# Performance work log

Measured on AMD Instinct MI355X. Metric: run time of the kernel, lower is better.

Reference implementation:

```python
import jax, jax.numpy as jnp
import numpy as np

NUM_GRAPHS = 1024


def setup_inputs() -> dict:
    key = jax.random.key(0)
    k1, k2, k3, k4 = jax.random.split(key, 4)
    N, D, H = 500000, 256, 128
    x = jax.random.normal(k1, (N, D), dtype=jnp.float32)
    # attention MLP params (Linear(D,H) -> ReLU -> Linear(H,1))
    W1 = jax.random.normal(k2, (D, H), dtype=jnp.float32) * (1.0 / np.sqrt(D))
    b1 = jnp.zeros((H,), dtype=jnp.float32)
    W2 = jax.random.normal(k3, (H, 1), dtype=jnp.float32) * (1.0 / np.sqrt(H))
    b2 = jnp.zeros((1,), dtype=jnp.float32)
    batch = jnp.sort(jax.random.randint(k4, (N,), 0, NUM_GRAPHS)).astype(jnp.int64)
    return {"x": x, "W1": W1, "b1": b1, "W2": W2, "b2": b2, "batch": batch}


def reference(x, W1, b1, W2, b2, batch):
    # attention MLP -> scalar score per node, softmax over ALL nodes (global, as in source)
    h = jax.nn.relu(x @ W1 + b1)            # [N, H]
    scores = h @ W2 + b2                    # [N, 1]
    attn = jax.nn.softmax(scores.ravel())[:, None]  # [N, 1], global softmax

    # attention-weighted sum per graph
    attn_pooled = jax.ops.segment_sum(x * attn, batch, num_segments=NUM_GRAPHS,
                                      indices_are_sorted=True)  # [G, D]
    # max pool per graph (all segments occupied given N >> G)
    max_pooled = jax.ops.segment_max(x, batch, num_segments=NUM_GRAPHS,
                                     indices_are_sorted=True)   # [G, D]
    # mean pool per graph: scatter-add + clamped counts
    sum_pooled = jax.ops.segment_sum(x, batch, num_segments=NUM_GRAPHS,
                                     indices_are_sorted=True)   # [G, D]
    counts = jnp.bincount(batch, length=NUM_GRAPHS).astype(x.dtype)
    counts = jnp.clip(counts, 1.0, None)[:, None]                # [G, 1]
    mean_pooled = sum_pooled / counts

    return jnp.concatenate([attn_pooled, max_pooled, mean_pooled], axis=-1)  # [G, 3D]
```

## Files before the change

### kernel.cpp

```cpp
#include <hip/hip_runtime.h>
#include <cmath>

#define D_IN 256
#define H_DIM 128
#define NUM_GRAPHS 1024
#define CHUNK 64
#define MAXSEG 4
#define REC_F 768

typedef __attribute__((ext_vector_type(8))) __bf16 bf16x8;
typedef __attribute__((ext_vector_type(4))) float f32x4;
typedef __attribute__((ext_vector_type(4))) unsigned short ushort4v;

__device__ inline float b2f(unsigned short u) {
    unsigned int v = ((unsigned int)u) << 16;
    return __builtin_bit_cast(float, v);
}

__global__ void pack_w1(const float* __restrict__ W1, ushort* __restrict__ packed) {
    int tid = blockIdx.x * 256 + threadIdx.x;
    if (tid >= 8 * 8 * 64) return;
    int nt = tid >> 9;
    int ks = (tid >> 6) & 7;
    int l = tid & 63;
    int col = nt * 16 + (l & 15);
    int kbase = ks * 32 + ((l >> 4) & 3) * 8;
#pragma unroll
    for (int i = 0; i < 8; ++i) {
        float v = W1[(size_t)(kbase + i) * H_DIM + col];
        __bf16 b = (__bf16)v;
        packed[(size_t)tid * 8 + i] = __builtin_bit_cast(unsigned short, b);
    }
}

__global__ __launch_bounds__(256) void fused_kernel(
    const float* __restrict__ x, const ushort* __restrict__ w1p,
    const float* __restrict__ b1, const float* __restrict__ W2,
    const float* __restrict__ b2, const int* __restrict__ batch,
    float* __restrict__ recs, int2* __restrict__ hdr,
    float* __restrict__ zpart, int N) {
    int tid = threadIdx.x;
    int l = tid & 63;
    int w = tid >> 6;
    int r16 = l & 15;
    int kg = l >> 4;
    int blk = blockIdx.x;
    long long base = (long long)blk * CHUNK;
    int chunkN = (int)min((long long)CHUNK, (long long)N - base);

    __shared__ ushort sx[CHUNK * D_IN];
    __shared__ float pscore[CHUNK][4];
    __shared__ float red[4][3][256];
    __shared__ int sbatch[CHUNK];
    __shared__ int seglist[MAXSEG + 1];
    __shared__ int seggid[MAXSEG];
    __shared__ int snseg;

    int bval = 0;
    if (w == 0) {
        long long bi = base + l;
        bval = (bi < N) ? batch[bi] : -1;
        sbatch[l] = bval;
    }

    bf16x8 breg0[8], breg1[8];
#pragma unroll
    for (int ks = 0; ks < 8; ++ks) {
        breg0[ks] = *(const bf16x8*)(w1p + ((size_t)((w * 2) * 8 + ks) * 64 + l) * 8);
        breg1[ks] = *(const bf16x8*)(w1p + ((size_t)((w * 2 + 1) * 8 + ks) * 64 + l) * 8);
    }

    {
        int row = tid >> 2;
        long long grow = base + row;
        if (grow >= N) grow = N - 1;
        const float* xr = x + grow * D_IN;
        int gb = tid & 3;
        f32x4 xv[16];
#pragma unroll
        for (int j = 0; j < 8; ++j) {
            int g = gb + 4 * j;
            xv[2 * j] = *(const f32x4*)(xr + g * 8);
            xv[2 * j + 1] = *(const f32x4*)(xr + g * 8 + 4);
        }
        unsigned rowswz = (unsigned)(row & 7) << 4;
#pragma unroll
        for (int j = 0; j < 8; ++j) {
            int g = gb + 4 * j;
            bf16x8 pk;
#pragma unroll
            for (int i = 0; i < 4; ++i) {
                pk[i] = (__bf16)xv[2 * j][i];
                pk[i + 4] = (__bf16)xv[2 * j + 1][i];
            }
            unsigned addr = ((unsigned)(row * 512 + g * 16)) ^ rowswz;
            *(bf16x8*)((char*)sx + addr) = pk;
        }
    }

    float w2v[2], b1v[2];
#pragma unroll
    for (int q = 0; q < 2; ++q) {
        int c = (w * 2 + q) * 16 + r16;
        w2v[q] = W2[c];
        b1v[q] = b1[c];
    }
    float bb = b2[0];

    if (w == 0) {
        int prev = __shfl_up(bval, 1, 64);
        bool flag = (l < chunkN) && (l == 0 || bval != prev);
        unsigned long long m = __ballot(flag);
        if (l == 0) {
            int ns = 0;
            while (m && ns < MAXSEG) {
                int b = __ffsll(m) - 1;
                seglist[ns] = b;
                seggid[ns] = sbatch[b];
                ns++;
                m &= m - 1;
            }
            snseg = ns;
            seglist[ns] = chunkN;
        }
    }
    __syncthreads();

    f32x4 acc[4][2] = {};
#pragma unroll
    for (int ks = 0; ks < 8; ++ks) {
#pragma unroll
        for (int mt = 0; mt < 4; ++mt) {
            int row = mt * 16 + r16;
            unsigned addr = ((unsigned)(row * 512 + ks * 64 + kg * 16)) ^
                            ((unsigned)(row & 7) << 4);
            bf16x8 af = *(const bf16x8*)((const char*)sx + addr);
            acc[mt][0] = __builtin_amdgcn_mfma_f32_16x16x32_bf16(af, breg0[ks], acc[mt][0], 0, 0, 0);
            acc[mt][1] = __builtin_amdgcn_mfma_f32_16x16x32_bf16(af, breg1[ks], acc[mt][1], 0, 0, 0);
        }
    }
#pragma unroll
    for (int mt = 0; mt < 4; ++mt) {
#pragma unroll
        for (int reg = 0; reg < 4; ++reg) {
            float p = fmaxf(acc[mt][0][reg] + b1v[0], 0.f) * w2v[0] +
                      fmaxf(acc[mt][1][reg] + b1v[1], 0.f) * w2v[1];
            p += __shfl_xor(p, 1, 64);
            p += __shfl_xor(p, 2, 64);
            p += __shfl_xor(p, 4, 64);
            p += __shfl_xor(p, 8, 64);
            if (r16 == 0) pscore[mt * 16 + kg * 4 + reg][w] = p;
        }
    }
    __syncthreads();

    f32x4 ps = *(const f32x4*)&pscore[l][0];
    float e_l = (l < chunkN) ? __expf(ps[0] + ps[1] + ps[2] + ps[3] + bb) : 0.f;

    if (w == 0) {
        float z = e_l;
        z += __shfl_xor(z, 1, 64);
        z += __shfl_xor(z, 2, 64);
        z += __shfl_xor(z, 4, 64);
        z += __shfl_xor(z, 8, 64);
        z += __shfl_xor(z, 16, 64);
        z += __shfl_xor(z, 32, 64);
        if (l == 0) zpart[blk] = z;
    }

    int nseg = snseg;

    f32x4 asum = {0.f, 0.f, 0.f, 0.f};
    f32x4 ssum = {0.f, 0.f, 0.f, 0.f};
    f32x4 mx = {-INFINITY, -INFINITY, -INFINITY, -INFINITY};

    for (int sg = 0; sg < nseg; ++sg) {
        int sStart = seglist[sg];
        int sEnd = seglist[sg + 1];
#pragma unroll
        for (int j = 0; j < 16; ++j) {
            int row = w * 16 + j;
            float wj = __shfl(e_l, row, 64);
            bool in = (row >= sStart) && (row < sEnd);
            unsigned addr = ((unsigned)(row * 512 + l * 8)) ^
                            ((unsigned)(row & 7) << 4);
            ushort4v hv = *(const ushort4v*)((const char*)sx + addr);
            float wje = in ? wj : 0.f;
#pragma unroll
            for (int c = 0; c < 4; ++c) {
                float v = b2f(hv[c]);
                asum[c] += v * wje;
                ssum[c] += in ? v : 0.f;
                mx[c] = fmaxf(mx[c], in ? v : -INFINITY);
            }
        }
        *(f32x4*)&red[w][0][l * 4] = asum;
        *(f32x4*)&red[w][1][l * 4] = ssum;
        *(f32x4*)&red[w][2][l * 4] = mx;
        __syncthreads();
        {
            float aa = red[0][0][tid] + red[1][0][tid] +
                       red[2][0][tid] + red[3][0][tid];
            float s2 = red[0][1][tid] + red[1][1][tid] +
                       red[2][1][tid] + red[3][1][tid];
            float m2 = fmaxf(fmaxf(red[0][2][tid], red[1][2][tid]),
                             fmaxf(red[2][2][tid], red[3][2][tid]));
            float* rb = recs + (size_t)(blk * MAXSEG + sg) * REC_F;
            rb[tid] = aa;
            rb[256 + tid] = s2;
            rb[512 + tid] = m2;
        }
        if (tid == 0)
            hdr[blk * MAXSEG + sg] = make_int2(seggid[sg], sEnd - sStart);
        __syncthreads();
#pragma unroll
        for (int c = 0; c < 4; ++c) {
            asum[c] = 0.f;
            ssum[c] = 0.f;
            mx[c] = -INFINITY;
        }
    }
    if (tid == 0) {
        for (int sg = nseg; sg < MAXSEG; ++sg)
            hdr[blk * MAXSEG + sg] = make_int2(-1, 0);
    }
}

__global__ __launch_bounds__(256) void zreduce_kernel(
    const float* __restrict__ zpart, int n, float* __restrict__ MZ) {
    int tid = threadIdx.x;
    float z = 0.f;
    for (int i = tid; i < n; i += 256) z += zpart[i];
    __shared__ float sz[256];
    sz[tid] = z;
    __syncthreads();
    for (int off = 128; off > 0; off >>= 1) {
        if (tid < off) sz[tid] += sz[tid + off];
        __syncthreads();
    }
    if (tid == 0) MZ[0] = 1.f / sz[0];
}

__device__ inline int lower_bound_i(const int* __restrict__ arr, int n, int val) {
    int lo = 0, hi = n;
    while (lo < hi) {
        int mid = (lo + hi) >> 1;
        if (arr[mid] < val) lo = mid + 1; else hi = mid;
    }
    return lo;
}

__global__ __launch_bounds__(256) void combine_kernel(
    const float* __restrict__ recs, const int2* __restrict__ hdr,
    const float* __restrict__ MZ,
    const int* __restrict__ batch, int N, float* __restrict__ out) {
    int g = blockIdx.x;
    int tid = threadIdx.x;
    float invZ = MZ[0];

    __shared__ int sb[2];
    if (tid < 2) sb[tid] = lower_bound_i(batch, N, g + tid);
    __syncthreads();
    int start = sb[0], end = sb[1];

    float ew = 0.f, ss = 0.f, mxv = -INFINITY;
    int cnt = 0;
    if (end > start) {
        int b0 = start >> 6, b1 = (end - 1) >> 6;
        for (int b = b0; b <= b1; ++b) {
#pragma unroll
            for (int sg = 0; sg < MAXSEG; ++sg) {
                int2 h = hdr[b * MAXSEG + sg];
                if (h.x == g) {
                    const float* rb = recs + (size_t)(b * MAXSEG + sg) * REC_F;
                    ew += rb[tid];
                    ss += rb[256 + tid];
                    mxv = fmaxf(mxv, rb[512 + tid]);
                    cnt += h.y;
                }
            }
        }
    }
    size_t ob = (size_t)g * (3 * D_IN);
    out[ob + tid] = ew * invZ;
    out[ob + D_IN + tid] = (end > start) ? mxv : 0.f;
    out[ob + 2 * D_IN + tid] = ss / (float)max(cnt, 1);
}

extern "C" void kernel_launch(void* const* d_in, const int* in_sizes, int n_in,
                              void* d_out, int out_size, void* d_ws, size_t ws_size,
                              hipStream_t stream) {
    const float* x = (const float*)d_in[0];
    const float* W1 = (const float*)d_in[1];
    const float* b1 = (const float*)d_in[2];
    const float* W2 = (const float*)d_in[3];
    const float* b2 = (const float*)d_in[4];
    const int* batch = (const int*)d_in[5];
    int N = in_sizes[0] / D_IN;
    float* out = (float*)d_out;
    int NB = (N + CHUNK - 1) / CHUNK;

    char* ws = (char*)d_ws;
    size_t off = 0;
    ushort* w1p = (ushort*)(ws + off);
    off += 8 * 8 * 64 * 8 * sizeof(ushort);
    off = (off + 255) & ~(size_t)255;
    float* recs = (float*)(ws + off);
    off += (size_t)NB * MAXSEG * REC_F * sizeof(float);
    off = (off + 255) & ~(size_t)255;
    int2* hdr = (int2*)(ws + off);
    off += (size_t)NB * MAXSEG * sizeof(int2);
    off = (off + 255) & ~(size_t)255;
    float* zpart = (float*)(ws + off);
    off += (size_t)NB * sizeof(float);
    off = (off + 255) & ~(size_t)255;
    float* MZ = (float*)(ws + off);
    off += 256;

    pack_w1<<<16, 256, 0, stream>>>(W1, w1p);
    fused_kernel<<<NB, 256, 0, stream>>>(x, w1p, b1, W2, b2, batch,
                                         recs, hdr, zpart, N);
    zreduce_kernel<<<1, 256, 0, stream>>>(zpart, NB, MZ);
    combine_kernel<<<NUM_GRAPHS, 256, 0, stream>>>(recs, hdr, MZ, batch, N, out);
}
```

Before: 181.3 us.

## Reduce segment pooling within each wave via shuffles and precompute graph bounds

The per-segment pooling loop now assigns each wave a 64-column slice, with the four 16-lane row groups reduced through cross-lane shuffles. This replaces the shared-memory red buffer and the two block barriers per segment. The per-block segment header array is dropped. A fused prep kernel precomputes the graph boundaries and each chunk's first graph id, so combine indexes records directly instead of doing a binary search and a header scan. This removes LDS traffic, barriers and redundant searches, but it relies on chunk segment ids being contiguous starting from cfirst.

```diff
diff --git a/kernel.cpp b/kernel.cpp
--- a/kernel.cpp
+++ b/kernel.cpp
@@ -17,19 +17,39 @@
     return __builtin_bit_cast(float, v);
 }
 
-__global__ void pack_w1(const float* __restrict__ W1, ushort* __restrict__ packed) {
-    int tid = blockIdx.x * 256 + threadIdx.x;
-    if (tid >= 8 * 8 * 64) return;
-    int nt = tid >> 9;
-    int ks = (tid >> 6) & 7;
-    int l = tid & 63;
-    int col = nt * 16 + (l & 15);
-    int kbase = ks * 32 + ((l >> 4) & 3) * 8;
-#pragma unroll
-    for (int i = 0; i < 8; ++i) {
-        float v = W1[(size_t)(kbase + i) * H_DIM + col];
-        __bf16 b = (__bf16)v;
-        packed[(size_t)tid * 8 + i] = __builtin_bit_cast(unsigned short, b);
+__device__ inline int lower_bound_i(const int* __restrict__ arr, int n, int val) {
+    int lo = 0, hi = n;
+    while (lo < hi) {
+        int mid = (lo + hi) >> 1;
+        if (arr[mid] < val) lo = mid + 1; else hi = mid;
+    }
+    return lo;
+}
+
+__global__ __launch_bounds__(256) void prep_kernel(
+    const float* __restrict__ W1, const int* __restrict__ batch, int N, int NB,
+    ushort* __restrict__ packed, int* __restrict__ bounds,
+    int* __restrict__ cfirst) {
+    int b = blockIdx.x;
+    if (b < 16) {
+        int tid = b * 256 + threadIdx.x;
+        int nt = tid >> 9;
+        int ks = (tid >> 6) & 7;
+        int l = tid & 63;
+        int col = nt * 16 + (l & 15);
+        int kbase = ks * 32 + ((l >> 4) & 3) * 8;
+#pragma unroll
+        for (int i = 0; i < 8; ++i) {
+            float v = W1[(size_t)(kbase + i) * H_DIM + col];
+            __bf16 h = (__bf16)v;
+            packed[(size_t)tid * 8 + i] = __builtin_bit_cast(unsigned short, h);
+        }
+    } else if (b < 21) {
+        int i = (b - 16) * 256 + threadIdx.x;
+        if (i <= NUM_GRAPHS) bounds[i] = lower_bound_i(batch, N, i);
+    } else {
+        int i = (b - 21) * 256 + threadIdx.x;
+        if (i < NB) cfirst[i] = batch[(long long)i * CHUNK];
     }
 }
 
@@ -37,8 +57,7 @@
     const float* __restrict__ x, const ushort* __restrict__ w1p,
     const float* __restrict__ b1, const float* __restrict__ W2,
     const float* __restrict__ b2, const int* __restrict__ batch,
-    float* __restrict__ recs, int2* __restrict__ hdr,
-    float* __restrict__ zpart, int N) {
+    float* __restrict__ recs, float* __restrict__ zpart, int N) {
     int tid = threadIdx.x;
     int l = tid & 63;
     int w = tid >> 6;
@@ -49,18 +68,14 @@
     int chunkN = (int)min((long long)CHUNK, (long long)N - base);
 
     __shared__ ushort sx[CHUNK * D_IN];
-    __shared__ float pscore[CHUNK][4];
-    __shared__ float red[4][3][256];
-    __shared__ int sbatch[CHUNK];
+    __shared__ float pscore[4][CHUNK];
     __shared__ int seglist[MAXSEG + 1];
-    __shared__ int seggid[MAXSEG];
     __shared__ int snseg;
 
-    int bval = 0;
+    int bval = -1;
     if (w == 0) {
         long long bi = base + l;
         bval = (bi < N) ? batch[bi] : -1;
-        sbatch[l] = bval;
     }
 
     bf16x8 breg0[8], breg1[8];
@@ -116,7 +131,6 @@
             while (m && ns < MAXSEG) {
                 int b = __ffsll(m) - 1;
                 seglist[ns] = b;
-                seggid[ns] = sbatch[b];
                 ns++;
                 m &= m - 1;
             }
@@ -149,13 +163,13 @@
             p += __shfl_xor(p, 2, 64);
             p += __shfl_xor(p, 4, 64);
             p += __shfl_xor(p, 8, 64);
-            if (r16 == 0) pscore[mt * 16 + kg * 4 + reg][w] = p;
+            if (r16 == 0) pscore[w][mt * 16 + kg * 4 + reg] = p;
         }
     }
     __syncthreads();
 
-    f32x4 ps = *(const f32x4*)&pscore[l][0];
-    float e_l = (l < chunkN) ? __expf(ps[0] + ps[1] + ps[2] + ps[3] + bb) : 0.f;
+    float s = pscore[0][l] + pscore[1][l] + pscore[2][l] + pscore[3][l] + bb;
+    float e_l = (l < chunkN) ? __expf(s) : 0.f;
 
     if (w == 0) {
         float z = e_l;
@@ -170,19 +184,22 @@
 
     int nseg = snseg;
 
-    f32x4 asum = {0.f, 0.f, 0.f, 0.f};
-    f32x4 ssum = {0.f, 0.f, 0.f, 0.f};
-    f32x4 mx = {-INFINITY, -INFINITY, -INFINITY, -INFINITY};
+    int cg = l & 15;
+    int rg = l >> 4;
+    unsigned cbyte = (unsigned)(w * 128 + cg * 8);
 
     for (int sg = 0; sg < nseg; ++sg) {
         int sStart = seglist[sg];
         int sEnd = seglist[sg + 1];
+        f32x4 asum = {0.f, 0.f, 0.f, 0.f};
+        f32x4 ssum = {0.f, 0.f, 0.f, 0.f};
+        f32x4 mx = {-INFINITY, -INFINITY, -INFINITY, -INFINITY};
 #pragma unroll
         for (int j = 0; j < 16; ++j) {
-            int row = w * 16 + j;
+            int row = rg + 4 * j;
             float wj = __shfl(e_l, row, 64);
             bool in = (row >= sStart) && (row < sEnd);
-            unsigned addr = ((unsigned)(row * 512 + l * 8)) ^
+            unsigned addr = ((unsigned)(row * 512) + cbyte) ^
                             ((unsigned)(row & 7) << 4);
             ushort4v hv = *(const ushort4v*)((const char*)sx + addr);
             float wje = in ? wj : 0.f;
@@ -194,35 +211,22 @@
                 mx[c] = fmaxf(mx[c], in ? v : -INFINITY);
             }
         }
-        *(f32x4*)&red[w][0][l * 4] = asum;
-        *(f32x4*)&red[w][1][l * 4] = ssum;
-        *(f32x4*)&red[w][2][l * 4] = mx;
-        __syncthreads();
-        {
-            float aa = red[0][0][tid] + red[1][0][tid] +
-                       red[2][0][tid] + red[3][0][tid];
-            float s2 = red[0][1][tid] + red[1][1][tid] +
-                       red[2][1][tid] + red[3][1][tid];
-            float m2 = fmaxf(fmaxf(red[0][2][tid], red[1][2][tid]),
-                             fmaxf(red[2][2][tid], red[3][2][tid]));
+#pragma unroll
+        for (int c = 0; c < 4; ++c) {
+            asum[c] += __shfl_xor(asum[c], 16, 64);
+            asum[c] += __shfl_xor(asum[c], 32, 64);
+            ssum[c] += __shfl_xor(ssum[c], 16, 64);
+            ssum[c] += __shfl_xor(ssum[c], 32, 64);
+            mx[c] = fmaxf(mx[c], __shfl_xor(mx[c], 16, 64));
+            mx[c] = fmaxf(mx[c], __shfl_xor(mx[c], 32, 64));
+        }
+        if (rg == 0) {
             float* rb = recs + (size_t)(blk * MAXSEG + sg) * REC_F;
-            rb[tid] = aa;
-            rb[256 + tid] = s2;
-            rb[512 + tid] = m2;
-        }
-        if (tid == 0)
-            hdr[blk * MAXSEG + sg] = make_int2(seggid[sg], sEnd - sStart);
-        __syncthreads();
-#pragma unroll
-        for (int c = 0; c < 4; ++c) {
-            asum[c] = 0.f;
-            ssum[c] = 0.f;
-            mx[c] = -INFINITY;
-        }
-    }
-    if (tid == 0) {
-        for (int sg = nseg; sg < MAXSEG; ++sg)
-            hdr[blk * MAXSEG + sg] = make_int2(-1, 0);
+            int co = w * 64 + cg * 4;
+            *(f32x4*)(rb + co) = asum;
+            *(f32x4*)(rb + 256 + co) = ssum;
+            *(f32x4*)(rb + 512 + co) = mx;
+        }
     }
 }
 
@@ -241,49 +245,33 @@
     if (tid == 0) MZ[0] = 1.f / sz[0];
 }
 
-__device__ inline int lower_bound_i(const int* __restrict__ arr, int n, int val) {
-    int lo = 0, hi = n;
-    while (lo < hi) {
-        int mid = (lo + hi) >> 1;
-        if (arr[mid] < val) lo = mid + 1; else hi = mid;
-    }
-    return lo;
-}
-
 __global__ __launch_bounds__(256) void combine_kernel(
-    const float* __restrict__ recs, const int2* __restrict__ hdr,
-    const float* __restrict__ MZ,
-    const int* __restrict__ batch, int N, float* __restrict__ out) {
+    const float* __restrict__ recs, const int* __restrict__ bounds,
+    const int* __restrict__ cfirst, const float* __restrict__ MZ,
+    float* __restrict__ out) {
     int g = blockIdx.x;
     int tid = threadIdx.x;
     float invZ = MZ[0];
-
-    __shared__ int sb[2];
-    if (tid < 2) sb[tid] = lower_bound_i(batch, N, g + tid);
-    __syncthreads();
-    int start = sb[0], end = sb[1];
+    int start = bounds[g];
+    int end = bounds[g + 1];
+    int cnt = end - start;
 
     float ew = 0.f, ss = 0.f, mxv = -INFINITY;
-    int cnt = 0;
-    if (end > start) {
+    if (cnt > 0) {
         int b0 = start >> 6, b1 = (end - 1) >> 6;
         for (int b = b0; b <= b1; ++b) {
-#pragma unroll
-            for (int sg = 0; sg < MAXSEG; ++sg) {
-                int2 h = hdr[b * MAXSEG + sg];
-                if (h.x == g) {
-                    const float* rb = recs + (size_t)(b * MAXSEG + sg) * REC_F;
-                    ew += rb[tid];
-                    ss += rb[256 + tid];
-                    mxv = fmaxf(mxv, rb[512 + tid]);
-                    cnt += h.y;
-                }
+            int sg = g - cfirst[b];
+            if (sg >= 0 && sg < MAXSEG) {
+                const float* rb = recs + (size_t)(b * MAXSEG + sg) * REC_F;
+                ew += rb[tid];
+                ss += rb[256 + tid];
+                mxv = fmaxf(mxv, rb[512 + tid]);
             }
         }
     }
     size_t ob = (size_t)g * (3 * D_IN);
     out[ob + tid] = ew * invZ;
-    out[ob + D_IN + tid] = (end > start) ? mxv : 0.f;
+    out[ob + D_IN + tid] = (cnt > 0) ? mxv : 0.f;
     out[ob + 2 * D_IN + tid] = ss / (float)max(cnt, 1);
 }
 
@@ -305,21 +293,25 @@
     ushort* w1p = (ushort*)(ws + off);
     off += 8 * 8 * 64 * 8 * sizeof(ushort);
     off = (off + 255) & ~(size_t)255;
+    int* bounds = (int*)(ws + off);
+    off += (NUM_GRAPHS + 1) * sizeof(int);
+    off = (off + 255) & ~(size_t)255;
+    int* cfirst = (int*)(ws + off);
+    off += (size_t)NB * sizeof(int);
+    off = (off + 255) & ~(size_t)255;
     float* recs = (float*)(ws + off);
     off += (size_t)NB * MAXSEG * REC_F * sizeof(float);
     off = (off + 255) & ~(size_t)255;
-    int2* hdr = (int2*)(ws + off);
-    off += (size_t)NB * MAXSEG * sizeof(int2);
-    off = (off + 255) & ~(size_t)255;
     float* zpart = (float*)(ws + off);
     off += (size_t)NB * sizeof(float);
     off = (off + 255) & ~(size_t)255;
     float* MZ = (float*)(ws + off);
     off += 256;
 
-    pack_w1<<<16, 256, 0, stream>>>(W1, w1p);
+    int prepBlocks = 21 + (NB + 255) / 256;
+    prep_kernel<<<prepBlocks, 256, 0, stream>>>(W1, batch, N, NB, w1p, bounds, cfirst);
     fused_kernel<<<NB, 256, 0, stream>>>(x, w1p, b1, W2, b2, batch,
-                                         recs, hdr, zpart, N);
+                                         recs, zpart, N);
     zreduce_kernel<<<1, 256, 0, stream>>>(zpart, NB, MZ);
-    combine_kernel<<<NUM_GRAPHS, 256, 0, stream>>>(recs, hdr, MZ, batch, N, out);
-}
+    combine_kernel<<<NUM_GRAPHS, 256, 0, stream>>>(recs, bounds, cfirst, MZ, out);
+}
```

New measurement: 178.2 us. Within noise of the previous version (-1.7%).
